# Kernel optimization log

Hardware: AMD Instinct MI355X
Metric: run time of the kernel (lower is better)

The kernel has to match this reference:

```python
import jax, jax.numpy as jnp
import numpy as np


def _gcn_conv(x, W, b, src, dst, dinv):
    # PyG GCNConv: linear transform, then symmetric-normalized aggregation, then bias
    n = x.shape[0]
    h = x @ W  # [N, out]
    norm = (dinv[src] * dinv[dst])[:, None]  # [E, 1]
    msg = h[src] * norm  # gather + scale, [E, out]
    out = jax.ops.segment_sum(msg, dst, num_segments=n)  # scatter-add
    return out + b


def setup_inputs() -> dict:
    key = jax.random.key(0)
    k1, k2, k3, k4 = jax.random.split(key, 4)
    N, E, F_IN, F_HID, F_OUT = 50000, 800000, 512, 256, 64
    x = jax.random.normal(k1, (N, F_IN), dtype=jnp.float32)
    edge_index = jax.random.randint(k2, (2, E), 0, N, dtype=jnp.int64)
    # Glorot-ish init for weights
    W1 = jax.random.normal(k3, (F_IN, F_HID), dtype=jnp.float32) * (1.0 / np.sqrt(F_IN))
    b1 = jnp.zeros((F_HID,), dtype=jnp.float32)
    W2 = jax.random.normal(k4, (F_HID, F_OUT), dtype=jnp.float32) * (1.0 / np.sqrt(F_HID))
    b2 = jnp.zeros((F_OUT,), dtype=jnp.float32)
    return {"x": x, "edge_index": edge_index, "W1": W1, "b1": b1, "W2": W2, "b2": b2}


def reference(x, edge_index, W1, b1, W2, b2):
    n = x.shape[0]
    # Add self loops (GCNConv default)
    loop = jnp.arange(n, dtype=edge_index.dtype)
    src = jnp.concatenate([edge_index[0], loop])
    dst = jnp.concatenate([edge_index[1], loop])
    # Symmetric normalization D^{-1/2} (A+I) D^{-1/2}
    deg = jax.ops.segment_sum(jnp.ones_like(dst, dtype=x.dtype), dst, num_segments=n)
    dinv = jnp.where(deg > 0, jax.lax.rsqrt(deg), 0.0)
    h = _gcn_conv(x, W1, b1, src, dst, dinv)
    h = jax.nn.relu(h)
    # Dropout(p=0.5) is identity in eval mode (deterministic reference)
    h = _gcn_conv(h, W2, b2, src, dst, dinv)
    return jax.nn.log_softmax(h, axis=1)
```

## Files before the change

kernel.cpp:

```cpp
#include <hip/hip_runtime.h>
#include <math.h>

#define F_IN  512
#define F_HID 256
#define F_OUT 64

typedef __attribute__((ext_vector_type(8))) short bf16x8;
typedef __attribute__((ext_vector_type(4))) short bf16x4;
typedef __attribute__((ext_vector_type(4))) float f32x4;

#define GLOBAL_AS __attribute__((address_space(1)))
#define LDS_AS    __attribute__((address_space(3)))

__device__ __forceinline__ void gload_lds16(const void* g, void* l) {
    __builtin_amdgcn_global_load_lds((const GLOBAL_AS uint32_t*)g,
                                     (LDS_AS uint32_t*)l, 16, 0, 0);
}

__device__ __forceinline__ ushort f2bf(float f) {
    union { float f; uint32_t u; } v; v.f = f;
    uint32_t r = (v.u + 0x7FFFu + ((v.u >> 16) & 1u)) >> 16;
    return (ushort)r;
}

__device__ __forceinline__ float bf2f(ushort u) {
    union { uint32_t u; float f; } v; v.u = ((uint32_t)u) << 16;
    return v.f;
}

__device__ __forceinline__ bf16x8 conv8(float4 a, float4 b) {
    bf16x8 c;
    c[0] = (short)f2bf(a.x); c[1] = (short)f2bf(a.y);
    c[2] = (short)f2bf(a.z); c[3] = (short)f2bf(a.w);
    c[4] = (short)f2bf(b.x); c[5] = (short)f2bf(b.y);
    c[6] = (short)f2bf(b.z); c[7] = (short)f2bf(b.w);
    return c;
}

__global__ void k_deg(const int* __restrict__ dst, int* __restrict__ deg, int E) {
    int e = blockIdx.x * 256 + threadIdx.x;
    if (e < E) atomicAdd(&deg[dst[e]], 1);
}

__global__ void k_scan1(const int* __restrict__ deg, int* __restrict__ offs,
                        int* __restrict__ bsums, float* __restrict__ dinv, int N) {
    __shared__ int s[256];
    int tid = threadIdx.x;
    int i = blockIdx.x * 256 + tid;
    int v = (i < N) ? deg[i] : 0;
    if (i < N) dinv[i] = rsqrtf((float)(v + 1));
    s[tid] = v; __syncthreads();
    for (int d = 1; d < 256; d <<= 1) {
        int t = (tid >= d) ? s[tid - d] : 0;
        __syncthreads();
        s[tid] += t;
        __syncthreads();
    }
    if (i < N) offs[i] = s[tid] - v;
    if (tid == 255) bsums[blockIdx.x] = s[255];
}

__global__ void k_scan2(int* __restrict__ bsums, int n) {
    __shared__ int s[256];
    int tid = threadIdx.x;
    int v = (tid < n) ? bsums[tid] : 0;
    s[tid] = v; __syncthreads();
    for (int d = 1; d < 256; d <<= 1) {
        int t = (tid >= d) ? s[tid - d] : 0;
        __syncthreads();
        s[tid] += t;
        __syncthreads();
    }
    if (tid < n) bsums[tid] = s[tid] - v;
}

__global__ void k_scan3(int* __restrict__ offs, const int* __restrict__ bsums,
                        int* __restrict__ cursor, int2* __restrict__ jw, int N, int E) {
    int i = blockIdx.x * 256 + threadIdx.x;
    if (i < N) {
        int o = offs[i] + bsums[i >> 8];
        offs[i] = o;
        cursor[i] = o;
    }
    if (i == 0) offs[N] = E;
    if (i < 32) jw[E + i] = make_int2(0, 0);
}

__global__ void k_fill(const int* __restrict__ src, const int* __restrict__ dst,
                       int* __restrict__ cursor, int2* __restrict__ jw,
                       const float* __restrict__ dinv, int E) {
    int e = blockIdx.x * 256 + threadIdx.x;
    if (e < E) {
        int s = src[e];
        int pos = atomicAdd(&cursor[dst[e]], 1);
        jw[pos] = make_int2(s, __float_as_int(dinv[s]));
    }
}

__global__ void k_tcast2(const float* __restrict__ W1, ushort* __restrict__ w1t,
                         const float* __restrict__ W2, ushort* __restrict__ w2t) {
    int idx = blockIdx.x * 256 + threadIdx.x;
    const int n1 = F_IN * F_HID;
    if (idx < n1) {
        int n = idx / F_IN, k = idx - n * F_IN;
        w1t[idx] = f2bf(W1[(size_t)k * F_HID + n]);
    } else {
        int t = idx - n1;
        if (t < F_HID * F_OUT) {
            int n = t / F_HID, k = t - n * F_HID;
            w2t[t] = f2bf(W2[(size_t)k * F_OUT + n]);
        }
    }
}

__global__ __launch_bounds__(256) void k_gemm1(
        const float* __restrict__ A, const ushort* __restrict__ Bt,
        ushort* __restrict__ C, int M, int nyblk) {
    constexpr int K = F_IN, Nc = F_HID, BM = 64, NT = K / 64;
    constexpr int ASTR = 72;
    __shared__ ushort As[2][BM * ASTR];
    __shared__ ushort Bs[2][128 * 64];
    const int tid  = threadIdx.x;
    const int wave = tid >> 6, lane = tid & 63;
    const int wr = wave & 1, wc = wave >> 1;
    const int l15 = lane & 15, hi = lane >> 4;

    int L = blockIdx.x;
    int nfull = (2 * nyblk) & ~15;
    int bx, by;
    if (L < nfull) { bx = (L >> 3) & 1; by = (L >> 4) * 8 + (L & 7); }
    else { int t = L - nfull; bx = t & 1; by = nfull / 2 + (t >> 1); }
    const int brow = by * BM, bcol = bx * 128;

    f32x4 acc[2][4];
    #pragma unroll
    for (int m = 0; m < 2; ++m)
        #pragma unroll
        for (int n = 0; n < 4; ++n) acc[m][n] = (f32x4){0.f, 0.f, 0.f, 0.f};

    const int arow = tid >> 2;
    const int akc  = (tid & 3) * 16;
    int agrow = brow + arow; if (agrow >= M) agrow = M - 1;
    const float4* ap = (const float4*)&A[(size_t)agrow * K + akc];
    const int bc = (lane & 7) ^ ((lane >> 3) & 7);
    const ushort* bp[4];
    int bdst[4];
    #pragma unroll
    for (int l = 0; l < 4; ++l) {
        int g = l * 4 + wave;
        int R = g * 8 + (lane >> 3);
        bp[l]   = &Bt[(size_t)(bcol + R) * K + bc * 8];
        bdst[l] = g * 512;
    }

    {
        float4 v0 = ap[0], v1 = ap[1], v2 = ap[2], v3 = ap[3];
        *(bf16x8*)&As[0][arow * ASTR + akc]     = conv8(v0, v1);
        *(bf16x8*)&As[0][arow * ASTR + akc + 8] = conv8(v2, v3);
        #pragma unroll
        for (int l = 0; l < 4; ++l) gload_lds16(bp[l], &Bs[0][bdst[l]]);
    }
    __syncthreads();

    #pragma unroll
    for (int t = 0; t < NT; ++t) {
        const int b = t & 1;
        if (t + 1 < NT) {
            #pragma unroll
            for (int l = 0; l < 4; ++l)
                gload_lds16(bp[l] + (t + 1) * 64, &Bs[b ^ 1][bdst[l]]);
            float4 v0 = ap[(t + 1) * 16], v1 = ap[(t + 1) * 16 + 1],
                   v2 = ap[(t + 1) * 16 + 2], v3 = ap[(t + 1) * 16 + 3];
            *(bf16x8*)&As[b ^ 1][arow * ASTR + akc]     = conv8(v0, v1);
            *(bf16x8*)&As[b ^ 1][arow * ASTR + akc + 8] = conv8(v2, v3);
        }
        #pragma unroll
        for (int ks = 0; ks < 2; ++ks) {
            const int kqA = ks * 32 + hi * 8;
            bf16x8 af[2], bfr[4];
            #pragma unroll
            for (int m = 0; m < 2; ++m)
                af[m] = *(const bf16x8*)&As[b][(wr * 32 + l15 + m * 16) * ASTR + kqA];
            #pragma unroll
            for (int n = 0; n < 4; ++n) {
                const int row = wc * 64 + l15 + n * 16;
                const int p = (ks * 4 + hi) ^ (l15 & 7);
                bfr[n] = *(const bf16x8*)&Bs[b][row * 64 + p * 8];
            }
            #pragma unroll
            for (int m = 0; m < 2; ++m)
                #pragma unroll
                for (int n = 0; n < 4; ++n)
                    acc[m][n] = __builtin_amdgcn_mfma_f32_16x16x32_bf16(af[m], bfr[n], acc[m][n], 0, 0, 0);
        }
        if (t + 1 < NT) __syncthreads();
    }

    const int crow0 = brow + wr * 32 + hi * 4;
    const int ccol0 = bcol + wc * 64 + l15;
    #pragma unroll
    for (int m = 0; m < 2; ++m)
        #pragma unroll
        for (int n = 0; n < 4; ++n)
            #pragma unroll
            for (int j = 0; j < 4; ++j) {
                int row = crow0 + m * 16 + j;
                if (row < M) C[(size_t)row * Nc + ccol0 + n * 16] = f2bf(acc[m][n][j]);
            }
}

template<int WR, int WC, int MR, int NR>
__global__ __launch_bounds__(256) void k_gemm_bf16(
        const ushort* __restrict__ A, const ushort* __restrict__ Bt,
        ushort* __restrict__ C, int M, int K, int Nc) {
    constexpr int BM = WR * MR * 16;
    constexpr int BN = WC * NR * 16;
    __shared__ ushort As[BM * 32];
    __shared__ ushort Bs[BN * 32];
    const int tid  = threadIdx.x;
    const int wave = tid >> 6, lane = tid & 63;
    const int wr = wave % WR, wc = wave / WR;
    const int brow = blockIdx.y * BM, bcol = blockIdx.x * BN;

    f32x4 acc[MR][NR];
    #pragma unroll
    for (int m = 0; m < MR; ++m)
        #pragma unroll
        for (int n = 0; n < NR; ++n) acc[m][n] = (f32x4){0.f, 0.f, 0.f, 0.f};

    const int srow = tid >> 2;
    const int scol = (tid & 3) * 8;
    const int kq  = (lane >> 4) * 8;
    const int rA0 = wr * MR * 16 + (lane & 15);
    const int rB0 = wc * NR * 16 + (lane & 15);

    for (int k0 = 0; k0 < K; k0 += 32) {
        #pragma unroll
        for (int l = 0; l < BM / 64; ++l) {
            int row = brow + l * 64 + srow;
            if (row >= M) row = M - 1;
            gload_lds16(&A[(size_t)row * K + k0 + scol], &As[l * 2048 + wave * 512]);
        }
        #pragma unroll
        for (int l = 0; l < BN / 64; ++l) {
            int row = bcol + l * 64 + srow;
            gload_lds16(&Bt[(size_t)row * K + k0 + scol], &Bs[l * 2048 + wave * 512]);
        }
        __syncthreads();
        bf16x8 af[MR], bfr[NR];
        #pragma unroll
        for (int m = 0; m < MR; ++m)
            af[m] = *(const bf16x8*)&As[(rA0 + m * 16) * 32 + kq];
        #pragma unroll
        for (int n = 0; n < NR; ++n)
            bfr[n] = *(const bf16x8*)&Bs[(rB0 + n * 16) * 32 + kq];
        #pragma unroll
        for (int m = 0; m < MR; ++m)
            #pragma unroll
            for (int n = 0; n < NR; ++n)
                acc[m][n] = __builtin_amdgcn_mfma_f32_16x16x32_bf16(af[m], bfr[n], acc[m][n], 0, 0, 0);
        __syncthreads();
    }

    const int crow0 = brow + wr * MR * 16 + (lane >> 4) * 4;
    const int ccol0 = bcol + wc * NR * 16 + (lane & 15);
    #pragma unroll
    for (int m = 0; m < MR; ++m)
        #pragma unroll
        for (int n = 0; n < NR; ++n)
            #pragma unroll
            for (int j = 0; j < 4; ++j) {
                int row = crow0 + m * 16 + j;
                if (row < M) C[(size_t)row * Nc + ccol0 + n * 16] = f2bf(acc[m][n][j]);
            }
}

__global__ __launch_bounds__(256) void k_agg1(
        const ushort* __restrict__ h, const int2* __restrict__ jw,
        const int* __restrict__ offs, const float* __restrict__ dinv,
        const float* __restrict__ bias, ushort* __restrict__ outm, int N) {
    int wave = threadIdx.x >> 6, lane = threadIdx.x & 63;
    int i = blockIdx.x * 4 + wave;
    if (i >= N) return;
    int g = lane & 31;
    int p = lane >> 5;
    float di = dinv[i];
    float acc[8];
    {
        bf16x8 hv = *(const bf16x8*)&h[(size_t)i * F_HID + g * 8];
        float w = (p == 0) ? di * di : 0.f;
        #pragma unroll
        for (int k = 0; k < 8; ++k) acc[k] = bf2f((ushort)hv[k]) * w;
    }
    int s = offs[i], e = offs[i + 1];
    for (int u = s; u < e; u += 16) {
        int2 a[8];
        #pragma unroll
        for (int q = 0; q < 8; ++q) a[q] = jw[u + 2 * q + p];
        bf16x8 hv[8];
        #pragma unroll
        for (int q = 0; q < 8; ++q)
            hv[q] = *(const bf16x8*)&h[(size_t)a[q].x * F_HID + g * 8];
        #pragma unroll
        for (int q = 0; q < 8; ++q) {
            float ww = (u + 2 * q + p < e) ? __int_as_float(a[q].y) * di : 0.f;
            #pragma unroll
            for (int k = 0; k < 8; ++k) acc[k] += bf2f((ushort)hv[q][k]) * ww;
        }
    }
    #pragma unroll
    for (int k = 0; k < 8; ++k) acc[k] += __shfl_xor(acc[k], 32, 64);
    if (p == 0) {
        float4 b0 = *(const float4*)&bias[g * 8];
        float4 b1 = *(const float4*)&bias[g * 8 + 4];
        bf16x8 o;
        o[0] = (short)f2bf(fmaxf(acc[0] + b0.x, 0.f));
        o[1] = (short)f2bf(fmaxf(acc[1] + b0.y, 0.f));
        o[2] = (short)f2bf(fmaxf(acc[2] + b0.z, 0.f));
        o[3] = (short)f2bf(fmaxf(acc[3] + b0.w, 0.f));
        o[4] = (short)f2bf(fmaxf(acc[4] + b1.x, 0.f));
        o[5] = (short)f2bf(fmaxf(acc[5] + b1.y, 0.f));
        o[6] = (short)f2bf(fmaxf(acc[6] + b1.z, 0.f));
        o[7] = (short)f2bf(fmaxf(acc[7] + b1.w, 0.f));
        *(bf16x8*)&outm[(size_t)i * F_HID + g * 8] = o;
    }
}

__global__ __launch_bounds__(256) void k_agg2(
        const ushort* __restrict__ h, const int2* __restrict__ jw,
        const int* __restrict__ offs, const float* __restrict__ dinv,
        const float* __restrict__ bias, float* __restrict__ outm, int N) {
    int wave = threadIdx.x >> 6, lane = threadIdx.x & 63;
    int i = blockIdx.x * 4 + wave;
    if (i >= N) return;
    int g4 = lane & 15;
    int p  = lane >> 4;
    float di = dinv[i];
    float acc[4];
    {
        bf16x4 hv = *(const bf16x4*)&h[(size_t)i * F_OUT + g4 * 4];
        float w = (p == 0) ? di * di : 0.f;
        #pragma unroll
        for (int k = 0; k < 4; ++k) acc[k] = bf2f((ushort)hv[k]) * w;
    }
    int s = offs[i], e = offs[i + 1];
    for (int u = s; u < e; u += 32) {
        int2 a[8];
        #pragma unroll
        for (int q = 0; q < 8; ++q) a[q] = jw[u + 4 * q + p];
        bf16x4 hv[8];
        #pragma unroll
        for (int q = 0; q < 8; ++q)
            hv[q] = *(const bf16x4*)&h[(size_t)a[q].x * F_OUT + g4 * 4];
        #pragma unroll
        for (int q = 0; q < 8; ++q) {
            float ww = (u + 4 * q + p < e) ? __int_as_float(a[q].y) * di : 0.f;
            #pragma unroll
            for (int k = 0; k < 4; ++k) acc[k] += bf2f((ushort)hv[q][k]) * ww;
        }
    }
    #pragma unroll
    for (int k = 0; k < 4; ++k) {
        acc[k] += __shfl_xor(acc[k], 16, 64);
        acc[k] += __shfl_xor(acc[k], 32, 64);
    }
    float4 bv = *(const float4*)&bias[g4 * 4];
    acc[0] += bv.x; acc[1] += bv.y; acc[2] += bv.z; acc[3] += bv.w;
    float m = fmaxf(fmaxf(acc[0], acc[1]), fmaxf(acc[2], acc[3]));
    #pragma unroll
    for (int o = 8; o >= 1; o >>= 1) m = fmaxf(m, __shfl_xor(m, o, 64));
    float ssum = expf(acc[0] - m) + expf(acc[1] - m) + expf(acc[2] - m) + expf(acc[3] - m);
    #pragma unroll
    for (int o = 8; o >= 1; o >>= 1) ssum += __shfl_xor(ssum, o, 64);
    float lse = m + logf(ssum);
    if (p == 0) {
        float4 o4;
        o4.x = acc[0] - lse; o4.y = acc[1] - lse;
        o4.z = acc[2] - lse; o4.w = acc[3] - lse;
        *(float4*)&outm[(size_t)i * F_OUT + g4 * 4] = o4;
    }
}

extern "C" void kernel_launch(void* const* d_in, const int* in_sizes, int n_in,
                              void* d_out, int out_size, void* d_ws, size_t ws_size,
                              hipStream_t stream) {
    const float* x  = (const float*)d_in[0];
    const int*   ei = (const int*)d_in[1];
    const float* W1 = (const float*)d_in[2];
    const float* b1 = (const float*)d_in[3];
    const float* W2 = (const float*)d_in[4];
    const float* b2 = (const float*)d_in[5];
    float* out = (float*)d_out;

    int N = in_sizes[0] / F_IN;
    int E = in_sizes[1] / 2;
    const int* src = ei;
    const int* dst = ei + E;

    ushort* w1t = (ushort*)d_ws;
    ushort* w2t = w1t + F_HID * F_IN;
    ushort* h1  = w2t + F_OUT * F_HID;
    ushort* a1  = h1 + (size_t)N * F_HID;
    int*    deg = (int*)(a1 + (size_t)N * F_HID);
    float*  dinv = (float*)(deg + N);
    int*    offs = (int*)(dinv + N);
    int*    cursor = offs + N + 1;
    int*    bsums  = cursor + N;
    int2*   jw = (int2*)(((uintptr_t)(bsums + 256) + 7) & ~(uintptr_t)7);
    ushort* h2 = h1;

    int nch = (N + 255) / 256;

    hipMemsetAsync(deg, 0, sizeof(int) * N, stream);
    k_deg <<<(E + 255) / 256, 256, 0, stream>>>(dst, deg, E);
    k_scan1<<<nch, 256, 0, stream>>>(deg, offs, bsums, dinv, N);
    k_scan2<<<1, 256, 0, stream>>>(bsums, nch);
    k_scan3<<<nch, 256, 0, stream>>>(offs, bsums, cursor, jw, N, E);
    k_fill<<<(E + 255) / 256, 256, 0, stream>>>(src, dst, cursor, jw, dinv, E);

    int ntc = F_IN * F_HID + F_HID * F_OUT;
    k_tcast2<<<(ntc + 255) / 256, 256, 0, stream>>>(W1, w1t, W2, w2t);

    int nyblk = (N + 63) / 64;
    k_gemm1<<<2 * nyblk, 256, 0, stream>>>(x, w1t, h1, N, nyblk);
    k_agg1<<<(N + 3) / 4, 256, 0, stream>>>(h1, jw, offs, dinv, b1, a1, N);

    k_gemm_bf16<4, 1, 1, 4><<<dim3(1, (N + 63) / 64), 256, 0, stream>>>(
        a1, w2t, h2, N, F_HID, F_OUT);
    k_agg2<<<(N + 3) / 4, 256, 0, stream>>>(h2, jw, offs, dinv, b2, out, N);
}
```

Measured before the change: 241.6 us.

## Fuse graph preprocessing into fewer launches with cooperative CSR build

After: 558.4 us. 131% more time.

```diff
diff --git a/kernel.cpp b/kernel.cpp
--- a/kernel.cpp
+++ b/kernel.cpp
@@ -1,4 +1,5 @@
 #include <hip/hip_runtime.h>
+#include <hip/hip_cooperative_groups.h>
 #include <math.h>
 
 #define F_IN  512
@@ -37,85 +38,88 @@
     return c;
 }
 
-__global__ void k_deg(const int* __restrict__ dst, int* __restrict__ deg, int E) {
-    int e = blockIdx.x * 256 + threadIdx.x;
-    if (e < E) atomicAdd(&deg[dst[e]], 1);
-}
-
-__global__ void k_scan1(const int* __restrict__ deg, int* __restrict__ offs,
-                        int* __restrict__ bsums, float* __restrict__ dinv, int N) {
+__global__ __launch_bounds__(256) void k_prep(
+        const float* __restrict__ W1, ushort* __restrict__ w1t,
+        const float* __restrict__ W2, ushort* __restrict__ w2t,
+        int* __restrict__ deg, int N) {
+    __shared__ ushort t[32][33];
+    int bid = blockIdx.x;
+    for (int i = bid * 256 + threadIdx.x; i < N; i += 144 * 256) deg[i] = 0;
+    const float* W; ushort* Wt; int K, Nc, tk, tn;
+    if (bid < 128) { W = W1; Wt = w1t; K = 512; Nc = 256; tk = bid >> 3; tn = bid & 7; }
+    else { int b = bid - 128; W = W2; Wt = w2t; K = 256; Nc = 64; tk = b >> 1; tn = b & 1; }
+    int r = threadIdx.x >> 5, c = threadIdx.x & 31;
+    #pragma unroll
+    for (int l = 0; l < 4; ++l)
+        t[r + l * 8][c] = f2bf(W[(size_t)(tk * 32 + r + l * 8) * Nc + tn * 32 + c]);
+    __syncthreads();
+    #pragma unroll
+    for (int l = 0; l < 4; ++l)
+        Wt[(size_t)(tn * 32 + r + l * 8) * K + tk * 32 + c] = t[c][r + l * 8];
+}
+
+__global__ __launch_bounds__(256) void k_csr(
+        const int* deg, int* offs, int* bsums, float* dinv,
+        int* cursor, int2* jw, const int* src, const int* dst,
+        int N, int E, int nch) {
+    namespace cg = cooperative_groups;
+    cg::grid_group grid = cg::this_grid();
     __shared__ int s[256];
     int tid = threadIdx.x;
-    int i = blockIdx.x * 256 + tid;
-    int v = (i < N) ? deg[i] : 0;
-    if (i < N) dinv[i] = rsqrtf((float)(v + 1));
-    s[tid] = v; __syncthreads();
-    for (int d = 1; d < 256; d <<= 1) {
-        int t = (tid >= d) ? s[tid - d] : 0;
-        __syncthreads();
-        s[tid] += t;
-        __syncthreads();
-    }
-    if (i < N) offs[i] = s[tid] - v;
-    if (tid == 255) bsums[blockIdx.x] = s[255];
-}
-
-__global__ void k_scan2(int* __restrict__ bsums, int n) {
-    __shared__ int s[256];
-    int tid = threadIdx.x;
-    int v = (tid < n) ? bsums[tid] : 0;
-    s[tid] = v; __syncthreads();
-    for (int d = 1; d < 256; d <<= 1) {
-        int t = (tid >= d) ? s[tid - d] : 0;
-        __syncthreads();
-        s[tid] += t;
-        __syncthreads();
-    }
-    if (tid < n) bsums[tid] = s[tid] - v;
-}
-
-__global__ void k_scan3(int* __restrict__ offs, const int* __restrict__ bsums,
-                        int* __restrict__ cursor, int2* __restrict__ jw, int N, int E) {
-    int i = blockIdx.x * 256 + threadIdx.x;
-    if (i < N) {
-        int o = offs[i] + bsums[i >> 8];
-        offs[i] = o;
-        cursor[i] = o;
-    }
-    if (i == 0) offs[N] = E;
-    if (i < 32) jw[E + i] = make_int2(0, 0);
-}
-
-__global__ void k_fill(const int* __restrict__ src, const int* __restrict__ dst,
-                       int* __restrict__ cursor, int2* __restrict__ jw,
-                       const float* __restrict__ dinv, int E) {
-    int e = blockIdx.x * 256 + threadIdx.x;
-    if (e < E) {
-        int s = src[e];
+    int bid = blockIdx.x;
+
+    if (bid < nch) {
+        int i = bid * 256 + tid;
+        int v = (i < N) ? deg[i] : 0;
+        if (i < N) dinv[i] = rsqrtf((float)(v + 1));
+        s[tid] = v; __syncthreads();
+        for (int d = 1; d < 256; d <<= 1) {
+            int t_ = (tid >= d) ? s[tid - d] : 0;
+            __syncthreads();
+            s[tid] += t_;
+            __syncthreads();
+        }
+        if (i < N) offs[i] = s[tid] - v;
+        if (tid == 255) bsums[bid] = s[255];
+    }
+    grid.sync();
+
+    if (bid == 0) {
+        int v = (tid < nch) ? bsums[tid] : 0;
+        s[tid] = v; __syncthreads();
+        for (int d = 1; d < 256; d <<= 1) {
+            int t_ = (tid >= d) ? s[tid - d] : 0;
+            __syncthreads();
+            s[tid] += t_;
+            __syncthreads();
+        }
+        if (tid < nch) bsums[tid] = s[tid] - v;
+    }
+    grid.sync();
+
+    if (bid < nch) {
+        int i = bid * 256 + tid;
+        if (i < N) {
+            int o = offs[i] + bsums[bid];
+            offs[i] = o;
+            cursor[i] = o;
+        }
+        if (i == 0) offs[N] = E;
+    }
+    if (bid == nch && tid < 32) jw[E + tid] = make_int2(0, 0);
+    grid.sync();
+
+    for (int e = bid * 256 + tid; e < E; e += gridDim.x * 256) {
+        int sj = src[e];
         int pos = atomicAdd(&cursor[dst[e]], 1);
-        jw[pos] = make_int2(s, __float_as_int(dinv[s]));
-    }
-}
-
-__global__ void k_tcast2(const float* __restrict__ W1, ushort* __restrict__ w1t,
-                         const float* __restrict__ W2, ushort* __restrict__ w2t) {
-    int idx = blockIdx.x * 256 + threadIdx.x;
-    const int n1 = F_IN * F_HID;
-    if (idx < n1) {
-        int n = idx / F_IN, k = idx - n * F_IN;
-        w1t[idx] = f2bf(W1[(size_t)k * F_HID + n]);
-    } else {
-        int t = idx - n1;
-        if (t < F_HID * F_OUT) {
-            int n = t / F_HID, k = t - n * F_HID;
-            w2t[t] = f2bf(W2[(size_t)k * F_OUT + n]);
-        }
+        jw[pos] = make_int2(sj, __float_as_int(dinv[sj]));
     }
 }
 
 __global__ __launch_bounds__(256) void k_gemm1(
         const float* __restrict__ A, const ushort* __restrict__ Bt,
-        ushort* __restrict__ C, int M, int nyblk) {
+        ushort* __restrict__ C, int M, int nyblk,
+        const int* __restrict__ dst, int* __restrict__ deg, int E) {
     constexpr int K = F_IN, Nc = F_HID, BM = 64, NT = K / 64;
     constexpr int ASTR = 72;
     __shared__ ushort As[2][BM * ASTR];
@@ -124,6 +128,13 @@
     const int wave = tid >> 6, lane = tid & 63;
     const int wr = wave & 1, wc = wave >> 1;
     const int l15 = lane & 15, hi = lane >> 4;
+
+    {
+        int e0 = blockIdx.x * 512 + tid;
+        if (e0 < E) atomicAdd(&deg[dst[e0]], 1);
+        int e1 = e0 + 256;
+        if (e1 < E) atomicAdd(&deg[dst[e1]], 1);
+    }
 
     int L = blockIdx.x;
     int nfull = (2 * nyblk) & ~15;
@@ -410,22 +421,23 @@
     ushort* h2 = h1;
 
     int nch = (N + 255) / 256;
-
-    hipMemsetAsync(deg, 0, sizeof(int) * N, stream);
-    k_deg <<<(E + 255) / 256, 256, 0, stream>>>(dst, deg, E);
-    k_scan1<<<nch, 256, 0, stream>>>(deg, offs, bsums, dinv, N);
-    k_scan2<<<1, 256, 0, stream>>>(bsums, nch);
-    k_scan3<<<nch, 256, 0, stream>>>(offs, bsums, cursor, jw, N, E);
-    k_fill<<<(E + 255) / 256, 256, 0, stream>>>(src, dst, cursor, jw, dinv, E);
-
-    int ntc = F_IN * F_HID + F_HID * F_OUT;
-    k_tcast2<<<(ntc + 255) / 256, 256, 0, stream>>>(W1, w1t, W2, w2t);
-
     int nyblk = (N + 63) / 64;
-    k_gemm1<<<2 * nyblk, 256, 0, stream>>>(x, w1t, h1, N, nyblk);
+
+    k_prep<<<144, 256, 0, stream>>>(W1, w1t, W2, w2t, deg, N);
+
+    k_gemm1<<<2 * nyblk, 256, 0, stream>>>(x, w1t, h1, N, nyblk, dst, deg, E);
+
+    {
+        void* args[] = {(void*)&deg, (void*)&offs, (void*)&bsums, (void*)&dinv,
+                        (void*)&cursor, (void*)&jw, (void*)&src, (void*)&dst,
+                        (void*)&N, (void*)&E, (void*)&nch};
+        hipLaunchCooperativeKernel((void*)k_csr, dim3(1024), dim3(256), args, 0, stream);
+    }
+
     k_agg1<<<(N + 3) / 4, 256, 0, stream>>>(h1, jw, offs, dinv, b1, a1, N);
 
     k_gemm_bf16<4, 1, 1, 4><<<dim3(1, (N + 63) / 64), 256, 0, stream>>>(
         a1, w2t, h2, N, F_HID, F_OUT);
+
     k_agg2<<<(N + 3) / 4, 256, 0, stream>>>(h2, jw, offs, dinv, b2, out, N);
 }
```

## Fuse degree counting into GEMM1 and merge memset with tiled weight transpose

Applied to the files above, without the earlier changes.

New measurement: 236.0 us. 2.3% less time.

```diff
diff --git a/kernel.cpp b/kernel.cpp
--- a/kernel.cpp
+++ b/kernel.cpp
@@ -37,9 +37,24 @@
     return c;
 }
 
-__global__ void k_deg(const int* __restrict__ dst, int* __restrict__ deg, int E) {
-    int e = blockIdx.x * 256 + threadIdx.x;
-    if (e < E) atomicAdd(&deg[dst[e]], 1);
+__global__ __launch_bounds__(256) void k_prep(
+        const float* __restrict__ W1, ushort* __restrict__ w1t,
+        const float* __restrict__ W2, ushort* __restrict__ w2t,
+        int* __restrict__ deg, int N) {
+    __shared__ ushort t[32][33];
+    int bid = blockIdx.x;
+    for (int i = bid * 256 + threadIdx.x; i < N; i += 144 * 256) deg[i] = 0;
+    const float* W; ushort* Wt; int K, Nc, tk, tn;
+    if (bid < 128) { W = W1; Wt = w1t; K = 512; Nc = 256; tk = bid >> 3; tn = bid & 7; }
+    else { int b = bid - 128; W = W2; Wt = w2t; K = 256; Nc = 64; tk = b >> 1; tn = b & 1; }
+    int r = threadIdx.x >> 5, c = threadIdx.x & 31;
+    #pragma unroll
+    for (int l = 0; l < 4; ++l)
+        t[r + l * 8][c] = f2bf(W[(size_t)(tk * 32 + r + l * 8) * Nc + tn * 32 + c]);
+    __syncthreads();
+    #pragma unroll
+    for (int l = 0; l < 4; ++l)
+        Wt[(size_t)(tn * 32 + r + l * 8) * K + tk * 32 + c] = t[c][r + l * 8];
 }
 
 __global__ void k_scan1(const int* __restrict__ deg, int* __restrict__ offs,
@@ -97,25 +112,10 @@
     }
 }
 
-__global__ void k_tcast2(const float* __restrict__ W1, ushort* __restrict__ w1t,
-                         const float* __restrict__ W2, ushort* __restrict__ w2t) {
-    int idx = blockIdx.x * 256 + threadIdx.x;
-    const int n1 = F_IN * F_HID;
-    if (idx < n1) {
-        int n = idx / F_IN, k = idx - n * F_IN;
-        w1t[idx] = f2bf(W1[(size_t)k * F_HID + n]);
-    } else {
-        int t = idx - n1;
-        if (t < F_HID * F_OUT) {
-            int n = t / F_HID, k = t - n * F_HID;
-            w2t[t] = f2bf(W2[(size_t)k * F_OUT + n]);
-        }
-    }
-}
-
 __global__ __launch_bounds__(256) void k_gemm1(
         const float* __restrict__ A, const ushort* __restrict__ Bt,
-        ushort* __restrict__ C, int M, int nyblk) {
+        ushort* __restrict__ C, int M, int nyblk,
+        const int* __restrict__ dst, int* __restrict__ deg, int E) {
     constexpr int K = F_IN, Nc = F_HID, BM = 64, NT = K / 64;
     constexpr int ASTR = 72;
     __shared__ ushort As[2][BM * ASTR];
@@ -124,6 +124,13 @@
     const int wave = tid >> 6, lane = tid & 63;
     const int wr = wave & 1, wc = wave >> 1;
     const int l15 = lane & 15, hi = lane >> 4;
+
+    {
+        int e0 = blockIdx.x * 512 + tid;
+        if (e0 < E) atomicAdd(&deg[dst[e0]], 1);
+        int e1 = e0 + 256;
+        if (e1 < E) atomicAdd(&deg[dst[e1]], 1);
+    }
 
     int L = blockIdx.x;
     int nfull = (2 * nyblk) & ~15;
@@ -410,22 +417,21 @@
     ushort* h2 = h1;
 
     int nch = (N + 255) / 256;
-
-    hipMemsetAsync(deg, 0, sizeof(int) * N, stream);
-    k_deg <<<(E + 255) / 256, 256, 0, stream>>>(dst, deg, E);
+    int nyblk = (N + 63) / 64;
+
+    k_prep<<<144, 256, 0, stream>>>(W1, w1t, W2, w2t, deg, N);
+
+    k_gemm1<<<2 * nyblk, 256, 0, stream>>>(x, w1t, h1, N, nyblk, dst, deg, E);
+
     k_scan1<<<nch, 256, 0, stream>>>(deg, offs, bsums, dinv, N);
     k_scan2<<<1, 256, 0, stream>>>(bsums, nch);
     k_scan3<<<nch, 256, 0, stream>>>(offs, bsums, cursor, jw, N, E);
     k_fill<<<(E + 255) / 256, 256, 0, stream>>>(src, dst, cursor, jw, dinv, E);
 
-    int ntc = F_IN * F_HID + F_HID * F_OUT;
-    k_tcast2<<<(ntc + 255) / 256, 256, 0, stream>>>(W1, w1t, W2, w2t);
-
-    int nyblk = (N + 63) / 64;
-    k_gemm1<<<2 * nyblk, 256, 0, stream>>>(x, w1t, h1, N, nyblk);
     k_agg1<<<(N + 3) / 4, 256, 0, stream>>>(h1, jw, offs, dinv, b1, a1, N);
 
     k_gemm_bf16<4, 1, 1, 4><<<dim3(1, (N + 63) / 64), 256, 0, stream>>>(
         a1, w2t, h2, N, F_HID, F_OUT);
+
     k_agg2<<<(N + 3) / 4, 256, 0, stream>>>(h2, jw, offs, dinv, b2, out, N);
 }
```
